# Optimization experiments

Hardware: AMD Instinct MI355X
Metric: run time of the kernel (lower is better)

The kernel has to match this reference:

```python
import math
import jax, jax.numpy as jnp
import numpy as np

N, D = 16384, 1024


def setup_inputs() -> dict:
    key = jax.random.key(0)
    k1, k2 = jax.random.split(key)
    return {
        "image_embeddings_aligned": jax.random.normal(k1, (N, D), dtype=jnp.float32),
        "text_embeddings_aligned": jax.random.normal(k2, (N, D), dtype=jnp.float32),
        "logit_scale": jnp.asarray(math.log(20.0), dtype=jnp.float32),  # stored as log(init)
        "logit_bias": jnp.asarray(-10.0, dtype=jnp.float32),
    }


def _l2_normalize(x, eps=1e-12):
    # matches F.normalize(p=2, dim=-1)
    n = jnp.linalg.norm(x, axis=-1, keepdims=True)
    return x / jnp.maximum(n, eps)


def reference(image_embeddings_aligned, text_embeddings_aligned, logit_scale, logit_bias):
    img = _l2_normalize(image_embeddings_aligned)
    txt = _l2_normalize(text_embeddings_aligned)
    # [N, N] pairwise logits
    logits = jnp.exp(logit_scale) * jnp.einsum("nd,md->nm", img, txt) + logit_bias
    n = logits.shape[0]
    labels = 2.0 * jnp.eye(n, dtype=logits.dtype) - 1.0  # +1 on diagonal, -1 off
    loss_matrix = jax.nn.log_sigmoid(labels * logits)
    siglip_loss = -jnp.mean(loss_matrix)  # total_loss (structure_lambda == 0)
    return siglip_loss
```

## Files before the change

### kernel.cpp

```cpp
#include <hip/hip_runtime.h>

#define NROWS 16384
#define DIM   1024
#define QSCALE 32.0f
#define E8M0S  0x7A7A7A7Au

typedef int    v4i    __attribute__((ext_vector_type(4)));
typedef int    v8i    __attribute__((ext_vector_type(8)));
typedef float  f32x16 __attribute__((ext_vector_type(16)));

__device__ __forceinline__ void glds16(const void* g, void* l) {
    __builtin_amdgcn_global_load_lds(
        (const __attribute__((address_space(1))) void*)g,
        (__attribute__((address_space(3))) void*)l,
        16, 0, 0);
}

__device__ __forceinline__ float fexp2(float x) {
#if __has_builtin(__builtin_amdgcn_exp2f)
    return __builtin_amdgcn_exp2f(x);
#else
    return exp2f(x);
#endif
}
__device__ __forceinline__ float flog2(float x) {
#if __has_builtin(__builtin_amdgcn_logf)
    return __builtin_amdgcn_logf(x);
#else
    return log2f(x);
#endif
}

__device__ __forceinline__ unsigned fp4_nib(float y) {
    unsigned s = (__float_as_uint(y) >> 31) << 3;
    float a = fminf(fabsf(y), 6.0f);
    unsigned c = (unsigned)(a >= 0.25f) + (unsigned)(a >= 0.75f) +
                 (unsigned)(a >= 1.25f) + (unsigned)(a >= 1.75f) +
                 (unsigned)(a >= 2.5f)  + (unsigned)(a >= 3.5f)  +
                 (unsigned)(a >= 5.0f);
    return c | s;
}

__global__ __launch_bounds__(256) void norm_fused(
    const float* __restrict__ img,
    const float* __restrict__ txt,
    unsigned char* __restrict__ imgQ,
    unsigned char* __restrict__ txtQ,
    const float* __restrict__ lscale,
    const float* __restrict__ lbias,
    float* __restrict__ diagPart) {
    const int t    = threadIdx.x;
    const int lane = t & 63;
    const int wave = t >> 6;
    const int gw   = blockIdx.x * 4 + wave;
    const float sc   = __expf(lscale[0]);
    const float bias = lbias[0];

    for (int row = gw; row < NROWS; row += 8192) {
        const float4* pi = (const float4*)(img + (size_t)row * DIM);
        const float4* pt = (const float4*)(txt + (size_t)row * DIM);
        float4 vi[4], vt[4];
        float ssi = 0.0f, sst = 0.0f, dot = 0.0f;
        #pragma unroll
        for (int j = 0; j < 4; ++j) {
            vi[j] = pi[lane + 64 * j];
            vt[j] = pt[lane + 64 * j];
            ssi += vi[j].x*vi[j].x + vi[j].y*vi[j].y + vi[j].z*vi[j].z + vi[j].w*vi[j].w;
            sst += vt[j].x*vt[j].x + vt[j].y*vt[j].y + vt[j].z*vt[j].z + vt[j].w*vt[j].w;
            dot += vi[j].x*vt[j].x + vi[j].y*vt[j].y + vi[j].z*vt[j].z + vi[j].w*vt[j].w;
        }
        #pragma unroll
        for (int off = 1; off < 64; off <<= 1) {
            ssi += __shfl_xor(ssi, off, 64);
            sst += __shfl_xor(sst, off, 64);
            dot += __shfl_xor(dot, off, 64);
        }
        const float ii = 1.0f / fmaxf(sqrtf(ssi), 1e-12f);
        const float it = 1.0f / fmaxf(sqrtf(sst), 1e-12f);
        if (lane == 0) diagPart[row] = -fmaf(sc, dot * ii * it, bias);

        const float qi = ii * QSCALE, qt = it * QSCALE;
        ushort* oi = (ushort*)(imgQ + (size_t)row * 512);
        ushort* ot = (ushort*)(txtQ + (size_t)row * 512);
        #pragma unroll
        for (int j = 0; j < 4; ++j) {
            unsigned p = fp4_nib(vi[j].x * qi)        | (fp4_nib(vi[j].y * qi) << 4) |
                         (fp4_nib(vi[j].z * qi) << 8) | (fp4_nib(vi[j].w * qi) << 12);
            unsigned q = fp4_nib(vt[j].x * qt)        | (fp4_nib(vt[j].y * qt) << 4) |
                         (fp4_nib(vt[j].z * qt) << 8) | (fp4_nib(vt[j].w * qt) << 12);
            oi[lane + 64 * j] = (ushort)p;
            ot[lane + 64 * j] = (ushort)q;
        }
    }
}

__global__ __launch_bounds__(512, 2) void siglip_gemm(
    const unsigned char* __restrict__ A,
    const unsigned char* __restrict__ B,
    const float* __restrict__ lscale,
    const float* __restrict__ lbias,
    float* __restrict__ gemmPart)
{
    __shared__ unsigned char sA[2][256 * 128];
    __shared__ unsigned char sB[2][256 * 128];
    __shared__ float wred[8];

    const int t    = threadIdx.x;
    const int lane = t & 63;
    const int wave = t >> 6;
    const int wr   = wave >> 2;
    const int wc   = wave & 3;
    const int r31  = lane & 31;
    const int h    = lane >> 5;
    const int xr   = (r31 & 7) ^ ((r31 >> 4) & 1);

    const int b    = blockIdx.x;
    const int xcd  = b & 7;
    const int lb   = b >> 3;
    const int bcol = xcd * 8 + (lb & 7);
    const int brow = lb >> 3;

    const size_t aBase = (size_t)brow * 256;
    const size_t bBase = (size_t)bcol * 256;

    const int srow = lane >> 3;
    const int c0   = (lane & 7) ^ srow;
    const int d01  = (c0 & 1) ? -16 : 16;

    const unsigned char* aP = A + (size_t)(aBase + wave * 32 + srow) * 512 + c0 * 16;
    const unsigned char* bP = B + (size_t)(bBase + wave * 32 + srow) * 512 + c0 * 16;

    int rbA[4], rbB[2];
    #pragma unroll
    for (int i = 0; i < 4; ++i) rbA[i] = (wr * 128 + i * 32 + r31) * 128;
    #pragma unroll
    for (int i = 0; i < 2; ++i) rbB[i] = (wc * 64 + i * 32 + r31) * 128;

    f32x16 acc[4][2] = {};

    {
        char* la = ((char*)sA[0]) + wave * 4096;
        char* lb_ = ((char*)sB[0]) + wave * 4096;
        #pragma unroll
        for (int j = 0; j < 4; ++j) {
            const int tog = ((j >> 1) & 1) ? d01 : 0;
            glds16(aP + j * 8 * 512 + tog, la + j * 1024);
            glds16(bP + j * 8 * 512 + tog, lb_ + j * 1024);
        }
    }

    #pragma unroll
    for (int k = 0; k < 4; ++k) {
        const int cur = k & 1;

        asm volatile("s_waitcnt vmcnt(0)" ::: "memory");
        __builtin_amdgcn_sched_barrier(0);
        __builtin_amdgcn_s_barrier();

        if (k < 3) {
            const unsigned char* aN = aP + (k + 1) * 128;
            const unsigned char* bN = bP + (k + 1) * 128;
            char* la = ((char*)sA[cur ^ 1]) + wave * 4096;
            char* lb_ = ((char*)sB[cur ^ 1]) + wave * 4096;
            #pragma unroll
            for (int j = 0; j < 4; ++j) {
                const int tog = ((j >> 1) & 1) ? d01 : 0;
                glds16(aN + j * 8 * 512 + tog, la + j * 1024);
                glds16(bN + j * 8 * 512 + tog, lb_ + j * 1024);
            }
        }

        v4i pa[2][4], pb[2][2];
        {
            const int s0 = (h ^ xr) * 16;
            #pragma unroll
            for (int i = 0; i < 4; ++i)
                pa[0][i] = *(const v4i*)(sA[cur] + rbA[i] + s0);
            #pragma unroll
            for (int n = 0; n < 2; ++n)
                pb[0][n] = *(const v4i*)(sB[cur] + rbB[n] + s0);
        }

        #pragma unroll
        for (int ks = 0; ks < 4; ++ks) {
            const int pc = ks & 1, pn = pc ^ 1;
            if (ks < 3) {
                const int s1 = (((ks + 1) * 2 + h) ^ xr) * 16;
                #pragma unroll
                for (int i = 0; i < 4; ++i)
                    pa[pn][i] = *(const v4i*)(sA[cur] + rbA[i] + s1);
                #pragma unroll
                for (int n = 0; n < 2; ++n)
                    pb[pn][n] = *(const v4i*)(sB[cur] + rbB[n] + s1);
                asm volatile("s_waitcnt lgkmcnt(6)" ::: "memory");
            } else {
                asm volatile("s_waitcnt lgkmcnt(0)" ::: "memory");
            }
            __builtin_amdgcn_sched_barrier(0);

            v8i a8[4], b8[2];
            #pragma unroll
            for (int i = 0; i < 4; ++i)
                a8[i] = __builtin_shufflevector(pa[pc][i], pa[pc][i],
                                                0, 1, 2, 3, -1, -1, -1, -1);
            #pragma unroll
            for (int n = 0; n < 2; ++n)
                b8[n] = __builtin_shufflevector(pb[pc][n], pb[pc][n],
                                                0, 1, 2, 3, -1, -1, -1, -1);

            __builtin_amdgcn_s_setprio(1);
            #pragma unroll
            for (int mi = 0; mi < 4; ++mi)
                #pragma unroll
                for (int ni = 0; ni < 2; ++ni)
                    acc[mi][ni] = __builtin_amdgcn_mfma_scale_f32_32x32x64_f8f6f4(
                        a8[mi], b8[ni], acc[mi][ni],
                        4, 4,
                        0, (int)E8M0S,
                        0, (int)E8M0S);
            __builtin_amdgcn_s_setprio(0);
        }
    }

    const float l2e   = 1.44269504088896341f;
    const float scale = __expf(lscale[0]);
    const float aCo   = scale * l2e;
    const float bCo   = lbias[0] * l2e;
    float local = 0.0f;
    #pragma unroll
    for (int mi = 0; mi < 4; ++mi)
        #pragma unroll
        for (int ni = 0; ni < 2; ++ni)
            #pragma unroll
            for (int r = 0; r < 16; r += 4) {
                float e0 = fexp2(fmaf(aCo, acc[mi][ni][r + 0], bCo));
                float e1 = fexp2(fmaf(aCo, acc[mi][ni][r + 1], bCo));
                float e2 = fexp2(fmaf(aCo, acc[mi][ni][r + 2], bCo));
                float e3 = fexp2(fmaf(aCo, acc[mi][ni][r + 3], bCo));
                float p  = ((1.0f + e0) * (1.0f + e1)) *
                           ((1.0f + e2) * (1.0f + e3));
                local += flog2(p);
            }

    #pragma unroll
    for (int off = 32; off > 0; off >>= 1) local += __shfl_down(local, off, 64);
    if (lane == 0) wred[wave] = local;
    __syncthreads();
    if (t == 0) {
        float tot = 0.0f;
        #pragma unroll
        for (int i = 0; i < 8; ++i) tot += wred[i];
        gemmPart[blockIdx.x] = tot * 0.69314718055994531f;
    }
}

__global__ __launch_bounds__(1024) void finalize_kernel(
    const float* __restrict__ parts, float* __restrict__ out) {
    __shared__ float wr[16];
    const int t    = threadIdx.x;
    const int lane = t & 63;
    const int wave = t >> 6;
    const float4* p4 = (const float4*)parts;
    float s = 0.0f;
    for (int i = t; i < 5120; i += 1024) {
        float4 v = p4[i];
        s += v.x + v.y + v.z + v.w;
    }
    #pragma unroll
    for (int off = 32; off > 0; off >>= 1) s += __shfl_down(s, off, 64);
    if (lane == 0) wr[wave] = s;
    __syncthreads();
    if (t == 0) {
        float tot = 0.0f;
        #pragma unroll
        for (int i = 0; i < 16; ++i) tot += wr[i];
        out[0] = tot / 268435456.0f;
    }
}

extern "C" void kernel_launch(void* const* d_in, const int* in_sizes, int n_in,
                              void* d_out, int out_size, void* d_ws, size_t ws_size,
                              hipStream_t stream) {
    const float* img    = (const float*)d_in[0];
    const float* txt    = (const float*)d_in[1];
    const float* lscale = (const float*)d_in[2];
    const float* lbias  = (const float*)d_in[3];
    float* out = (float*)d_out;

    char* ws = (char*)d_ws;
    unsigned char* imgQ = (unsigned char*)ws;
    unsigned char* txtQ = (unsigned char*)(ws + (size_t)NROWS * 512);
    float* parts   = (float*)(ws + (size_t)2 * NROWS * 512);
    float* diagPart = parts;
    float* gemmPart = parts + NROWS;

    norm_fused<<<2048, 256, 0, stream>>>(img, txt, imgQ, txtQ, lscale, lbias, diagPart);
    siglip_gemm<<<dim3((NROWS / 256) * (NROWS / 256)), 512, 0, stream>>>(
        imgQ, txtQ, lscale, lbias, gemmPart);
    finalize_kernel<<<1, 1024, 0, stream>>>(parts, out);
}
```

Before: 312.7 us.

## Make siglip GEMM persistent with cross-tile prefetch and interleaved LDS staging

Launches 256 persistent blocks instead of 4096. Each block loops over 16 output tiles (2 row tiles by 8 column tiles) and prefetches the next tile's first K-slice while it finishes the current one. Global-to-LDS loads are spread across the MFMA sub-steps rather than issued in one burst, and the barrier moves to the end of each K step. The goal is to hide tile prologue and epilogue latency and launch overhead. The cost is a fixed grid of 256 blocks, which may not fill every CU, and serialized per-tile epilogues inside each block. The finalize loop count changes to match the smaller number of partial sums.

```diff
diff --git a/kernel.cpp b/kernel.cpp
--- a/kernel.cpp
+++ b/kernel.cpp
@@ -114,21 +114,12 @@
     const int h    = lane >> 5;
     const int xr   = (r31 & 7) ^ ((r31 >> 4) & 1);
 
-    const int b    = blockIdx.x;
-    const int xcd  = b & 7;
-    const int lb   = b >> 3;
-    const int bcol = xcd * 8 + (lb & 7);
-    const int brow = lb >> 3;
-
-    const size_t aBase = (size_t)brow * 256;
-    const size_t bBase = (size_t)bcol * 256;
+    const int blk = blockIdx.x;
 
     const int srow = lane >> 3;
     const int c0   = (lane & 7) ^ srow;
     const int d01  = (c0 & 1) ? -16 : 16;
-
-    const unsigned char* aP = A + (size_t)(aBase + wave * 32 + srow) * 512 + c0 * 16;
-    const unsigned char* bP = B + (size_t)(bBase + wave * 32 + srow) * 512 + c0 * 16;
+    const int off0 = (wave * 32 + srow) * 512 + c0 * 16;
 
     int rbA[4], rbB[2];
     #pragma unroll
@@ -138,109 +129,145 @@
 
     f32x16 acc[4][2] = {};
 
+    const float l2e   = 1.44269504088896341f;
+    const float aCo   = __expf(lscale[0]) * l2e;
+    const float bCo   = lbias[0] * l2e;
+    float local = 0.0f;
+
     {
+        const unsigned char* a0 = A + (size_t)((blk >> 3) * 2) * 131072 + off0;
+        const unsigned char* b0 = B + (size_t)((blk & 7) * 8) * 131072 + off0;
         char* la = ((char*)sA[0]) + wave * 4096;
-        char* lb_ = ((char*)sB[0]) + wave * 4096;
-        #pragma unroll
-        for (int j = 0; j < 4; ++j) {
-            const int tog = ((j >> 1) & 1) ? d01 : 0;
-            glds16(aP + j * 8 * 512 + tog, la + j * 1024);
-            glds16(bP + j * 8 * 512 + tog, lb_ + j * 1024);
+        char* lb = ((char*)sB[0]) + wave * 4096;
+        glds16(a0,                la);
+        glds16(a0 + 4096,         la + 1024);
+        glds16(a0 + 8192  + d01,  la + 2048);
+        glds16(a0 + 12288 + d01,  la + 3072);
+        glds16(b0,                lb);
+        glds16(b0 + 4096,         lb + 1024);
+        glds16(b0 + 8192  + d01,  lb + 2048);
+        glds16(b0 + 12288 + d01,  lb + 3072);
+        asm volatile("s_waitcnt vmcnt(0)" ::: "memory");
+    }
+    __builtin_amdgcn_s_barrier();
+
+    for (int tile = 0; tile < 16; ++tile) {
+        const int browC = (blk >> 3) * 2 + (tile >> 3);
+        const int bcolC = (blk & 7) * 8 + (tile & 7);
+        const int tN    = (tile + 1) & 15;
+        const int browN = (blk >> 3) * 2 + (tN >> 3);
+        const int bcolN = (blk & 7) * 8 + (tN & 7);
+
+        const unsigned char* aCur = A + (size_t)browC * 131072 + off0;
+        const unsigned char* bCur = B + (size_t)bcolC * 131072 + off0;
+        const unsigned char* aNxt = A + (size_t)browN * 131072 + off0;
+        const unsigned char* bNxt = B + (size_t)bcolN * 131072 + off0;
+
+        #pragma unroll
+        for (int k = 0; k < 4; ++k) {
+            const int cur = k & 1;
+            const unsigned char* gA = (k < 3 ? aCur + (k + 1) * 128 : aNxt);
+            const unsigned char* gB = (k < 3 ? bCur + (k + 1) * 128 : bNxt);
+            const bool doStage = (k < 3) || (tile < 15);
+            char* laN = ((char*)sA[cur ^ 1]) + wave * 4096;
+            char* lbN = ((char*)sB[cur ^ 1]) + wave * 4096;
+
+            v4i pa[2][4], pb[2][2];
+            {
+                const int s0 = (h ^ xr) * 16;
+                #pragma unroll
+                for (int i = 0; i < 4; ++i)
+                    pa[0][i] = *(const v4i*)(sA[cur] + rbA[i] + s0);
+                #pragma unroll
+                for (int n = 0; n < 2; ++n)
+                    pb[0][n] = *(const v4i*)(sB[cur] + rbB[n] + s0);
+            }
+
+            #pragma unroll
+            for (int ks = 0; ks < 4; ++ks) {
+                const int pc = ks & 1, pn = pc ^ 1;
+                if (ks < 3) {
+                    const int s1 = (((ks + 1) * 2 + h) ^ xr) * 16;
+                    #pragma unroll
+                    for (int i = 0; i < 4; ++i)
+                        pa[pn][i] = *(const v4i*)(sA[cur] + rbA[i] + s1);
+                    #pragma unroll
+                    for (int n = 0; n < 2; ++n)
+                        pb[pn][n] = *(const v4i*)(sB[cur] + rbB[n] + s1);
+                    asm volatile("s_waitcnt lgkmcnt(6)" ::: "memory");
+                } else {
+                    asm volatile("s_waitcnt lgkmcnt(0)" ::: "memory");
+                }
+                __builtin_amdgcn_sched_barrier(0);
+
+                if (doStage) {
+                    if (ks == 0) {
+                        glds16(gA,               laN);
+                        glds16(gA + 4096,        laN + 1024);
+                    } else if (ks == 1) {
+                        glds16(gA + 8192  + d01, laN + 2048);
+                        glds16(gA + 12288 + d01, laN + 3072);
+                    } else if (ks == 2) {
+                        glds16(gB,               lbN);
+                        glds16(gB + 4096,        lbN + 1024);
+                    } else {
+                        glds16(gB + 8192  + d01, lbN + 2048);
+                        glds16(gB + 12288 + d01, lbN + 3072);
+                    }
+                }
+                __builtin_amdgcn_sched_barrier(0);
+
+                v8i a8[4], b8[2];
+                #pragma unroll
+                for (int i = 0; i < 4; ++i)
+                    a8[i] = __builtin_shufflevector(pa[pc][i], pa[pc][i],
+                                                    0, 1, 2, 3, -1, -1, -1, -1);
+                #pragma unroll
+                for (int n = 0; n < 2; ++n)
+                    b8[n] = __builtin_shufflevector(pb[pc][n], pb[pc][n],
+                                                    0, 1, 2, 3, -1, -1, -1, -1);
+
+                __builtin_amdgcn_s_setprio(1);
+                #pragma unroll
+                for (int mi = 0; mi < 4; ++mi)
+                    #pragma unroll
+                    for (int ni = 0; ni < 2; ++ni)
+                        acc[mi][ni] = __builtin_amdgcn_mfma_scale_f32_32x32x64_f8f6f4(
+                            a8[mi], b8[ni], acc[mi][ni],
+                            4, 4,
+                            0, (int)E8M0S,
+                            0, (int)E8M0S);
+                __builtin_amdgcn_s_setprio(0);
+            }
+
+            if (k < 3) {
+                asm volatile("s_waitcnt vmcnt(0)" ::: "memory");
+                __builtin_amdgcn_sched_barrier(0);
+                __builtin_amdgcn_s_barrier();
+            }
         }
-    }
-
-    #pragma unroll
-    for (int k = 0; k < 4; ++k) {
-        const int cur = k & 1;
+
+        #pragma unroll
+        for (int mi = 0; mi < 4; ++mi)
+            #pragma unroll
+            for (int ni = 0; ni < 2; ++ni) {
+                #pragma unroll
+                for (int r = 0; r < 16; r += 4) {
+                    float e0 = fexp2(fmaf(aCo, acc[mi][ni][r + 0], bCo));
+                    float e1 = fexp2(fmaf(aCo, acc[mi][ni][r + 1], bCo));
+                    float e2 = fexp2(fmaf(aCo, acc[mi][ni][r + 2], bCo));
+                    float e3 = fexp2(fmaf(aCo, acc[mi][ni][r + 3], bCo));
+                    float p  = ((1.0f + e0) * (1.0f + e1)) *
+                               ((1.0f + e2) * (1.0f + e3));
+                    local += flog2(p);
+                }
+                acc[mi][ni] = (f32x16)0.0f;
+            }
 
         asm volatile("s_waitcnt vmcnt(0)" ::: "memory");
         __builtin_amdgcn_sched_barrier(0);
         __builtin_amdgcn_s_barrier();
-
-        if (k < 3) {
-            const unsigned char* aN = aP + (k + 1) * 128;
-            const unsigned char* bN = bP + (k + 1) * 128;
-            char* la = ((char*)sA[cur ^ 1]) + wave * 4096;
-            char* lb_ = ((char*)sB[cur ^ 1]) + wave * 4096;
-            #pragma unroll
-            for (int j = 0; j < 4; ++j) {
-                const int tog = ((j >> 1) & 1) ? d01 : 0;
-                glds16(aN + j * 8 * 512 + tog, la + j * 1024);
-                glds16(bN + j * 8 * 512 + tog, lb_ + j * 1024);
-            }
-        }
-
-        v4i pa[2][4], pb[2][2];
-        {
-            const int s0 = (h ^ xr) * 16;
-            #pragma unroll
-            for (int i = 0; i < 4; ++i)
-                pa[0][i] = *(const v4i*)(sA[cur] + rbA[i] + s0);
-            #pragma unroll
-            for (int n = 0; n < 2; ++n)
-                pb[0][n] = *(const v4i*)(sB[cur] + rbB[n] + s0);
-        }
-
-        #pragma unroll
-        for (int ks = 0; ks < 4; ++ks) {
-            const int pc = ks & 1, pn = pc ^ 1;
-            if (ks < 3) {
-                const int s1 = (((ks + 1) * 2 + h) ^ xr) * 16;
-                #pragma unroll
-                for (int i = 0; i < 4; ++i)
-                    pa[pn][i] = *(const v4i*)(sA[cur] + rbA[i] + s1);
-                #pragma unroll
-                for (int n = 0; n < 2; ++n)
-                    pb[pn][n] = *(const v4i*)(sB[cur] + rbB[n] + s1);
-                asm volatile("s_waitcnt lgkmcnt(6)" ::: "memory");
-            } else {
-                asm volatile("s_waitcnt lgkmcnt(0)" ::: "memory");
-            }
-            __builtin_amdgcn_sched_barrier(0);
-
-            v8i a8[4], b8[2];
-            #pragma unroll
-            for (int i = 0; i < 4; ++i)
-                a8[i] = __builtin_shufflevector(pa[pc][i], pa[pc][i],
-                                                0, 1, 2, 3, -1, -1, -1, -1);
-            #pragma unroll
-            for (int n = 0; n < 2; ++n)
-                b8[n] = __builtin_shufflevector(pb[pc][n], pb[pc][n],
-                                                0, 1, 2, 3, -1, -1, -1, -1);
-
-            __builtin_amdgcn_s_setprio(1);
-            #pragma unroll
-            for (int mi = 0; mi < 4; ++mi)
-                #pragma unroll
-                for (int ni = 0; ni < 2; ++ni)
-                    acc[mi][ni] = __builtin_amdgcn_mfma_scale_f32_32x32x64_f8f6f4(
-                        a8[mi], b8[ni], acc[mi][ni],
-                        4, 4,
-                        0, (int)E8M0S,
-                        0, (int)E8M0S);
-            __builtin_amdgcn_s_setprio(0);
-        }
-    }
-
-    const float l2e   = 1.44269504088896341f;
-    const float scale = __expf(lscale[0]);
-    const float aCo   = scale * l2e;
-    const float bCo   = lbias[0] * l2e;
-    float local = 0.0f;
-    #pragma unroll
-    for (int mi = 0; mi < 4; ++mi)
-        #pragma unroll
-        for (int ni = 0; ni < 2; ++ni)
-            #pragma unroll
-            for (int r = 0; r < 16; r += 4) {
-                float e0 = fexp2(fmaf(aCo, acc[mi][ni][r + 0], bCo));
-                float e1 = fexp2(fmaf(aCo, acc[mi][ni][r + 1], bCo));
-                float e2 = fexp2(fmaf(aCo, acc[mi][ni][r + 2], bCo));
-                float e3 = fexp2(fmaf(aCo, acc[mi][ni][r + 3], bCo));
-                float p  = ((1.0f + e0) * (1.0f + e1)) *
-                           ((1.0f + e2) * (1.0f + e3));
-                local += flog2(p);
-            }
+    }
 
     #pragma unroll
     for (int off = 32; off > 0; off >>= 1) local += __shfl_down(local, off, 64);
@@ -250,7 +277,7 @@
         float tot = 0.0f;
         #pragma unroll
         for (int i = 0; i < 8; ++i) tot += wred[i];
-        gemmPart[blockIdx.x] = tot * 0.69314718055994531f;
+        gemmPart[blk] = tot * 0.69314718055994531f;
     }
 }
 
@@ -262,7 +289,7 @@
     const int wave = t >> 6;
     const float4* p4 = (const float4*)parts;
     float s = 0.0f;
-    for (int i = t; i < 5120; i += 1024) {
+    for (int i = t; i < 4160; i += 1024) {
         float4 v = p4[i];
         s += v.x + v.y + v.z + v.w;
     }
@@ -295,7 +322,6 @@
     float* gemmPart = parts + NROWS;
 
     norm_fused<<<2048, 256, 0, stream>>>(img, txt, imgQ, txtQ, lscale, lbias, diagPart);
-    siglip_gemm<<<dim3((NROWS / 256) * (NROWS / 256)), 512, 0, stream>>>(
-        imgQ, txtQ, lscale, lbias, gemmPart);
+    siglip_gemm<<<256, 512, 0, stream>>>(imgQ, txtQ, lscale, lbias, gemmPart);
     finalize_kernel<<<1, 1024, 0, stream>>>(parts, out);
 }
```

New measurement: 897.8 us. 187% more time.
